# Optimization experiments

Hardware: AMD Instinct MI355X
Metric: run time of the kernel (lower is better)

## Reference

```python
import jax, jax.numpy as jnp
from jax import lax
import numpy as np

PN_FEAT = 64


def _conv(x, w, b):
    # x: [B,H,W,Cin], w: [kh,kw,Cin,Cout] (SAME padding, stride 1)
    return lax.conv_general_dilated(x, w, (1, 1), 'SAME',
                                    dimension_numbers=('NHWC', 'HWIO', 'NHWC')) + b


def setup_inputs() -> dict:
    key = jax.random.key(0)
    ks = jax.random.split(key, 12)
    B, P, N, C = 4, 5000, 100, 8
    nx = ny = 240
    pillars = jax.random.normal(ks[0], (B, P, N, C), dtype=jnp.float32)
    pillar_idxs = jax.random.randint(ks[1], (B, P, 2), 0, nx).astype(jnp.int32)
    def lin(k, fi, fo):
        return jax.random.normal(k, (fi, fo), dtype=jnp.float32) / np.sqrt(fi).astype(np.float32)
    def cnv(k, kh, kw, ci, co):
        return jax.random.normal(k, (kh, kw, ci, co), dtype=jnp.float32) / np.sqrt(kh * kw * ci).astype(np.float32)
    return {
        'pillars': pillars,
        'pillar_idxs': pillar_idxs,
        'nx': nx,
        'ny': ny,
        # pointnet MLP: 8 -> 64 (tanh) -> 64
        'pn_w0': lin(ks[2], 8, 64), 'pn_b0': jnp.zeros((64,), jnp.float32),
        'pn_w1': lin(ks[3], 64, PN_FEAT), 'pn_b1': jnp.zeros((PN_FEAT,), jnp.float32),
        # resnet costmap CNN: 64 -> 128 (tanh) -> 128 (tanh) -> 1, relu output
        'cw0': cnv(ks[4], 3, 3, PN_FEAT, 128), 'cb0': jnp.zeros((128,), jnp.float32),
        'cw1': cnv(ks[5], 3, 3, 128, 128), 'cb1': jnp.zeros((128,), jnp.float32),
        'cw2': cnv(ks[6], 1, 1, 128, 1), 'cb2': jnp.zeros((1,), jnp.float32),
    }


def reference(pillars, pillar_idxs, nx, ny,
              pn_w0, pn_b0, pn_w1, pn_b1,
              cw0, cb0, cw1, cb1, cw2, cb2):
    VALID_THRESH = 1000000.0
    ACT_SCALE = 1.0
    # mask padded points (norm >= 1e6 means invalid)
    valid = (jnp.linalg.norm(pillars, axis=-1, keepdims=True) < VALID_THRESH).astype(pillars.dtype)
    # per-point MLP: [B,P,N,8] -> [B,P,N,F]
    h = jnp.tanh(pillars @ pn_w0 + pn_b0)
    feat = h @ pn_w1 + pn_b1
    # masked max over points in each pillar -> [B,P,F]
    pmax = jnp.max(feat * valid, axis=-2)
    # scatter pillar features into BEV pseudo-image [B,nx,ny,F]
    B = pillars.shape[0]
    bidx = jnp.arange(B)[:, None]                      # [B,1]
    img = jnp.zeros((B, nx, ny, PN_FEAT), pillars.dtype)
    img = img.at[bidx, pillar_idxs[..., 0], pillar_idxs[..., 1]].set(pmax)
    # costmap CNN head (NHWC internally; original is NCHW, same math)
    x = jnp.tanh(_conv(img, cw0, cb0))
    x = jnp.tanh(_conv(x, cw1, cb1))
    x = _conv(x, cw2, cb2)
    return jax.nn.relu(x) * ACT_SCALE            # [B,nx,ny,1]
```

## Files before the change

kernel.cpp:

```cpp
#include <hip/hip_runtime.h>
#include <hip/hip_bf16.h>
#include <math.h>

#define B  4
#define P  5000
#define NPT 100
#define F  64
#define NX 240
#define NY 240
#define C1 128

typedef __attribute__((ext_vector_type(8)))  short short8;
typedef __attribute__((ext_vector_type(16))) float f32x16;

__device__ __forceinline__ float tanh_fast(float x) {
    float e = __expf(2.0f * x);
    float r = __builtin_amdgcn_rcpf(e + 1.0f);
    return __builtin_fmaf(-2.0f, r, 1.0f);
}
__device__ __forceinline__ short bf16_bits(float f) {
    return (short)(__bfloat16_as_ushort(__float2bfloat16(f)));
}

__global__ __launch_bounds__(128) void pn_mfma_kernel(
    const float* __restrict__ pillars,
    const short* __restrict__ w0p,
    const float* __restrict__ b0,
    const __hip_bfloat16* __restrict__ w1t,
    const float* __restrict__ b1,
    float* __restrict__ pmax)
{
    constexpr int HS = F + 8;
    constexpr int XS = 40;
    __shared__ short xA[128 * XS];
    __shared__ short hA[128 * HS];
    __shared__ float red[2][F];
    __shared__ unsigned int vb32[4];

    int bp = blockIdx.x;
    int n  = threadIdx.x;
    int wave = n >> 6, lane = n & 63;
    int mr = lane & 31;
    int g  = lane >> 5;
    bool live = (n < NPT);

    const float* xp = pillars + ((size_t)bp * NPT + (live ? n : 0)) * 8;
    float4 q0 = *(const float4*)xp;
    float4 q1 = *(const float4*)(xp + 4);
    float x[8] = {q0.x, q0.y, q0.z, q0.w, q1.x, q1.y, q1.z, q1.w};

    float ss = 0.f;
#pragma unroll
    for (int c = 0; c < 8; c++) ss += x[c] * x[c];
    bool valid = live && (ss < 1e12f);

    unsigned long long bal = __ballot(valid);
    if (lane == 0) {
        vb32[wave * 2]     = (unsigned)bal;
        vb32[wave * 2 + 1] = (unsigned)(bal >> 32);
    }

    short8 xhi, xlo, xz;
#pragma unroll
    for (int c = 0; c < 8; c++) {
        __hip_bfloat16 hb = __float2bfloat16(x[c]);
        float hv = __bfloat162float(hb);
        xhi[c] = (short)__bfloat16_as_ushort(hb);
        xlo[c] = bf16_bits(x[c] - hv);
        xz[c] = 0;
    }
    *(short8*)&xA[n * XS + 0]  = xhi;
    *(short8*)&xA[n * XS + 8]  = xlo;
    *(short8*)&xA[n * XS + 16] = xhi;
    *(short8*)&xA[n * XS + 24] = xz;
    __syncthreads();

    short8 wb[2][2];
#pragma unroll
    for (int kk = 0; kk < 2; kk++)
#pragma unroll
        for (int nt = 0; nt < 2; nt++)
            wb[kk][nt] = *(const short8*)(w0p + ((kk * 2 + g) * 64 + nt * 32 + mr) * 8);

    f32x16 hc00 = {0,0,0,0,0,0,0,0,0,0,0,0,0,0,0,0};
    f32x16 hc01 = hc00, hc10 = hc00, hc11 = hc00;
#pragma unroll
    for (int kk = 0; kk < 2; kk++) {
        short8 a0 = *(const short8*)&xA[(wave * 64 + mr) * XS + kk * 16 + g * 8];
        short8 a1 = *(const short8*)&xA[(wave * 64 + 32 + mr) * XS + kk * 16 + g * 8];
        hc00 = __builtin_amdgcn_mfma_f32_32x32x16_bf16(a0, wb[kk][0], hc00, 0, 0, 0);
        hc01 = __builtin_amdgcn_mfma_f32_32x32x16_bf16(a0, wb[kk][1], hc01, 0, 0, 0);
        hc10 = __builtin_amdgcn_mfma_f32_32x32x16_bf16(a1, wb[kk][0], hc10, 0, 0, 0);
        hc11 = __builtin_amdgcn_mfma_f32_32x32x16_bf16(a1, wb[kk][1], hc11, 0, 0, 0);
    }

    float b00 = b0[mr];
    float b01 = b0[32 + mr];
#pragma unroll
    for (int mt = 0; mt < 2; mt++) {
#pragma unroll
        for (int r = 0; r < 16; r++) {
            int prow = wave * 64 + mt * 32 + (r & 3) + 8 * (r >> 2) + 4 * g;
            float h0 = (mt == 0) ? hc00[r] : hc10[r];
            float h1 = (mt == 0) ? hc01[r] : hc11[r];
            hA[prow * HS + mr]      = bf16_bits(tanh_fast(h0 + b00));
            hA[prow * HS + 32 + mr] = bf16_bits(tanh_fast(h1 + b01));
        }
    }
    __syncthreads();

    short8 bfrag[2][4];
#pragma unroll
    for (int nt = 0; nt < 2; nt++)
#pragma unroll
        for (int c0 = 0; c0 < 4; c0++)
            bfrag[nt][c0] = *(const short8*)((const short*)w1t +
                                (nt * 32 + mr) * F + c0 * 16 + g * 8);

    f32x16 acc00 = {0,0,0,0,0,0,0,0,0,0,0,0,0,0,0,0};
    f32x16 acc01 = acc00, acc10 = acc00, acc11 = acc00;

    const short* arow = &hA[(wave * 64 + mr) * HS + g * 8];
#pragma unroll
    for (int c0 = 0; c0 < 4; c0++) {
        short8 af0 = *(const short8*)(arow + c0 * 16);
        short8 af1 = *(const short8*)(arow + 32 * HS + c0 * 16);
        acc00 = __builtin_amdgcn_mfma_f32_32x32x16_bf16(af0, bfrag[0][c0], acc00, 0, 0, 0);
        acc01 = __builtin_amdgcn_mfma_f32_32x32x16_bf16(af0, bfrag[1][c0], acc01, 0, 0, 0);
        acc10 = __builtin_amdgcn_mfma_f32_32x32x16_bf16(af1, bfrag[0][c0], acc10, 0, 0, 0);
        acc11 = __builtin_amdgcn_mfma_f32_32x32x16_bf16(af1, bfrag[1][c0], acc11, 0, 0, 0);
    }

    float bv0 = b1[mr];
    float bv1 = b1[32 + mr];
    bool allv = ((vb32[0] & vb32[1] & vb32[2]) == 0xFFFFFFFFu) &&
                ((vb32[3] & 0xFu) == 0xFu);
    float mx0 = -INFINITY, mx1 = -INFINITY;

    if (allv) {
#pragma unroll
        for (int mt = 0; mt < 2; mt++) {
#pragma unroll
            for (int r = 0; r < 16; r++) {
                bool inc = !(wave == 1 && mt == 1) || (g == 0 && r < 4);
                if (inc) {
                    mx0 = fmaxf(mx0, (mt == 0) ? acc00[r] : acc10[r]);
                    mx1 = fmaxf(mx1, (mt == 0) ? acc01[r] : acc11[r]);
                }
            }
        }
        mx0 += bv0;
        mx1 += bv1;
    } else {
        unsigned wm0 = vb32[wave * 2];
        unsigned wm1 = vb32[wave * 2 + 1];
#pragma unroll
        for (int mt = 0; mt < 2; mt++) {
            unsigned wm = (mt == 0) ? wm0 : wm1;
#pragma unroll
            for (int r = 0; r < 16; r++) {
                int idx = (r & 3) + 8 * (r >> 2) + 4 * g;
                bool inc = !(wave == 1 && mt == 1) || (idx < 4);
                if (inc) {
                    bool vbit = (wm >> idx) & 1;
                    float a0 = (mt == 0) ? acc00[r] : acc10[r];
                    float a1 = (mt == 0) ? acc01[r] : acc11[r];
                    mx0 = fmaxf(mx0, vbit ? (a0 + bv0) : 0.0f);
                    mx1 = fmaxf(mx1, vbit ? (a1 + bv1) : 0.0f);
                }
            }
        }
    }
    mx0 = fmaxf(mx0, __shfl_xor(mx0, 32, 64));
    mx1 = fmaxf(mx1, __shfl_xor(mx1, 32, 64));
    if (lane < 32) { red[wave][mr] = mx0; red[wave][32 + mr] = mx1; }
    __syncthreads();
    if (n < F)
        pmax[(size_t)bp * F + n] = fmaxf(red[0][n], red[1][n]);
}

__global__ __launch_bounds__(256) void winner_kernel(
    const int* __restrict__ idxs, int* __restrict__ winner)
{
    int i = blockIdx.x * 256 + threadIdx.x;
    if (i >= B * P) return;
    int ix = idxs[i * 2], iy = idxs[i * 2 + 1];
    int b = i / P, p = i % P;
    atomicMax(&winner[(b * NX + ix) * NY + iy], p);
}

__global__ __launch_bounds__(64) void scatter_kernel(
    const int* __restrict__ idxs, const int* __restrict__ winner,
    const float* __restrict__ pmax, __hip_bfloat16* __restrict__ img)
{
    int bp = blockIdx.x;
    int f = threadIdx.x;
    int ix = idxs[bp * 2], iy = idxs[bp * 2 + 1];
    int b = bp / P, p = bp % P;
    int cell = (b * NX + ix) * NY + iy;
    if (winner[cell] == p)
        img[(size_t)cell * F + f] = __float2bfloat16(pmax[(size_t)bp * F + f]);
}

__global__ __launch_bounds__(256) void cvt_w_kernel(
    const float* __restrict__ w, __hip_bfloat16* __restrict__ wt, int cin)
{
    int idx = blockIdx.x * 256 + threadIdx.x;
    int total = 9 * cin * 128;
    if (idx >= total) return;
    int co = idx % 128;
    int rest = idx / 128;
    int ci = rest % cin;
    int t  = rest / cin;
    int c0 = ci >> 4, c16 = ci & 15;
    wt[(((size_t)(t * (cin >> 4) + c0)) * 128 + co) * 16 + c16] = __float2bfloat16(w[idx]);
}

__global__ __launch_bounds__(256) void cvt_w1_kernel(
    const float* __restrict__ w1, __hip_bfloat16* __restrict__ w1t)
{
    int idx = blockIdx.x * 256 + threadIdx.x;
    if (idx >= F * F) return;
    int k = idx >> 6, nn = idx & 63;
    w1t[nn * F + k] = __float2bfloat16(w1[idx]);
}

__global__ __launch_bounds__(256) void cvt_w0p_kernel(
    const float* __restrict__ w0, short* __restrict__ w0p)
{
    int idx = blockIdx.x * 256 + threadIdx.x;
    if (idx >= 4 * 64 * 8) return;
    int j = idx & 7;
    int nn = (idx >> 3) & 63;
    int s = idx >> 9;
    float wv = w0[j * F + nn];
    __hip_bfloat16 hb = __float2bfloat16(wv);
    short out = 0;
    if (s < 2)      out = (short)__bfloat16_as_ushort(hb);
    else if (s == 2) out = bf16_bits(wv - __bfloat162float(hb));
    w0p[idx] = out;
}

template<int CIN, bool FUSE>
__global__ __launch_bounds__(256, 2) void conv_mfma(
    const __hip_bfloat16* __restrict__ in,
    const __hip_bfloat16* __restrict__ wt,
    const float* __restrict__ bias,
    const float* __restrict__ w2,
    const float* __restrict__ b2,
    __hip_bfloat16* __restrict__ out_bf,
    float* __restrict__ out_f)
{
    constexpr int PASSES = CIN / 64;
    constexpr int CI   = 64;
    constexpr int CPAD = CI + 8;
    constexpr int NC16 = CI / 16;
    constexpr int NC8  = CI / 8;
    constexpr int ROWS = 4 * 130;
    __shared__ short sP[ROWS * CPAD];
    __shared__ float sred[FUSE ? 2 : 1][2][128];

    int tid  = threadIdx.x;
    int wave = tid >> 6;
    int lane = tid & 63;
    int mr = lane & 31;
    int g  = lane >> 5;
    int coh = wave & 1;
    int xr  = wave >> 1;
    int x0 = blockIdx.x * 2;
    int y0 = blockIdx.y * 112;
    int b  = blockIdx.z;
    int n0 = coh * 64;

    const short* wts = (const short*)wt;

    f32x16 acc[4][2];
#pragma unroll
    for (int mt = 0; mt < 4; mt++)
#pragma unroll
        for (int nt = 0; nt < 2; nt++)
            acc[mt][nt] = (f32x16){0,0,0,0,0,0,0,0,0,0,0,0,0,0,0,0};

    short8 wbuf[2][NC16][2];
#pragma unroll
    for (int c0 = 0; c0 < NC16; c0++)
#pragma unroll
        for (int nt = 0; nt < 2; nt++)
            wbuf[0][c0][nt] = *(const short8*)(wts +
                ((0 * (CIN / 16) + c0) * 128 + n0 + nt * 32 + mr) * 16 + g * 8);

#pragma unroll
    for (int p = 0; p < PASSES; p++) {
        if (p) __syncthreads();

#pragma unroll 4
        for (int i = 0; i < 17; i++) {
            int t = tid + i * 256;
            if (t < ROWS * NC8) {
                int c8 = t & (NC8 - 1);
                int r  = t >> 3;
                int dx = r / 130, dy = r - dx * 130;
                int gx = x0 - 1 + dx, gy = y0 - 1 + dy;
                float4 v = make_float4(0.f, 0.f, 0.f, 0.f);
                if (gx >= 0 && gx < NX && gy >= 0 && gy < NY)
                    v = *(const float4*)&in[(((size_t)b * NX + gx) * NY + gy) * CIN + p * CI + c8 * 8];
                *(float4*)&sP[r * CPAD + c8 * 8] = v;
            }
        }
        __syncthreads();

#pragma unroll
        for (int tap = 0; tap < 9; tap++) {
            int s = p * 9 + tap;
            int cur = s & 1;
            if (s + 1 < 9 * PASSES) {
                int sn = s + 1, pn_ = sn / 9, tn = sn % 9;
#pragma unroll
                for (int c0 = 0; c0 < NC16; c0++)
#pragma unroll
                    for (int nt = 0; nt < 2; nt++)
                        wbuf[cur ^ 1][c0][nt] = *(const short8*)(wts +
                            ((tn * (CIN / 16) + pn_ * NC16 + c0) * 128 + n0 + nt * 32 + mr) * 16 + g * 8);
            }
            int kh = tap / 3, kw = tap % 3;
            const short* abase = sP + ((xr + kh) * 130 + kw + mr) * CPAD + g * 8;
#pragma unroll
            for (int c0 = 0; c0 < NC16; c0++) {
                short8 a[4];
#pragma unroll
                for (int mt = 0; mt < 4; mt++)
                    a[mt] = *(const short8*)(abase + mt * 32 * CPAD + c0 * 16);
#pragma unroll
                for (int mt = 0; mt < 4; mt++) {
                    acc[mt][0] = __builtin_amdgcn_mfma_f32_32x32x16_bf16(a[mt], wbuf[cur][c0][0], acc[mt][0], 0, 0, 0);
                    acc[mt][1] = __builtin_amdgcn_mfma_f32_32x32x16_bf16(a[mt], wbuf[cur][c0][1], acc[mt][1], 0, 0, 0);
                }
            }
        }
    }

    float bv0 = bias[n0 + mr];
    float bv1 = bias[n0 + 32 + mr];
    if (!FUSE) {
        size_t base = ((size_t)b * NX + (x0 + xr)) * NY;
#pragma unroll
        for (int mt = 0; mt < 4; mt++) {
#pragma unroll
            for (int r = 0; r < 16; r++) {
                int y = y0 + mt * 32 + (r & 3) + 8 * (r >> 2) + 4 * g;
                out_bf[(base + y) * C1 + n0 + mr]      = __float2bfloat16(tanh_fast(acc[mt][0][r] + bv0));
                out_bf[(base + y) * C1 + n0 + 32 + mr] = __float2bfloat16(tanh_fast(acc[mt][1][r] + bv1));
            }
        }
    } else {
        float w20 = w2[n0 + mr];
        float w21 = w2[n0 + 32 + mr];
#pragma unroll
        for (int mt = 0; mt < 4; mt++) {
#pragma unroll
            for (int r = 0; r < 16; r++) {
                float v = tanh_fast(acc[mt][0][r] + bv0) * w20
                        + tanh_fast(acc[mt][1][r] + bv1) * w21;
                v += __shfl_xor(v, 1, 64);
                v += __shfl_xor(v, 2, 64);
                v += __shfl_xor(v, 4, 64);
                v += __shfl_xor(v, 8, 64);
                v += __shfl_xor(v, 16, 64);
                if (mr == 0)
                    sred[coh][xr][mt * 32 + (r & 3) + 8 * (r >> 2) + 4 * g] = v;
            }
        }
        __syncthreads();
        {
            int row = tid & 127;
            int xr2 = tid >> 7;
            float r = sred[0][xr2][row] + sred[1][xr2][row] + b2[0];
            out_f[((size_t)b * NX + (x0 + xr2)) * NY + (y0 + row)] = fmaxf(r, 0.f);
        }
    }
}

extern "C" void kernel_launch(void* const* d_in, const int* in_sizes, int n_in,
                              void* d_out, int out_size, void* d_ws, size_t ws_size,
                              hipStream_t stream) {
    const float* pillars = (const float*)d_in[0];
    const int*   idxs    = (const int*)d_in[1];
    const float* pn_w0   = (const float*)d_in[4];
    const float* pn_b0   = (const float*)d_in[5];
    const float* pn_w1   = (const float*)d_in[6];
    const float* pn_b1   = (const float*)d_in[7];
    const float* cw0     = (const float*)d_in[8];
    const float* cb0     = (const float*)d_in[9];
    const float* cw1     = (const float*)d_in[10];
    const float* cb1     = (const float*)d_in[11];
    const float* cw2     = (const float*)d_in[12];
    const float* cb2     = (const float*)d_in[13];
    float* out = (float*)d_out;

    char* ws = (char*)d_ws;
    const size_t IMG_BYTES  = (size_t)B * NX * NY * F * 2;
    const size_t OUT1_BYTES = (size_t)B * NX * NY * C1 * 2;
    const size_t WIN_BYTES  = (size_t)B * NX * NY * 4;
    const size_t PMAX_BYTES = (size_t)B * P * F * 4;
    const size_t WT1_BYTES  = (size_t)9 * C1 * F * 2;
    const size_t WT2_BYTES  = (size_t)9 * C1 * C1 * 2;
    const size_t W1T_BYTES  = (size_t)F * F * 2;
    __hip_bfloat16* img  = (__hip_bfloat16*)ws;
    __hip_bfloat16* out1 = (__hip_bfloat16*)(ws + IMG_BYTES);
    int*   winner = (int*)(ws + IMG_BYTES + OUT1_BYTES);
    float* pmax   = (float*)(ws + IMG_BYTES + OUT1_BYTES + WIN_BYTES);
    __hip_bfloat16* wt1 = (__hip_bfloat16*)(ws + IMG_BYTES + OUT1_BYTES + WIN_BYTES + PMAX_BYTES);
    __hip_bfloat16* wt2 = (__hip_bfloat16*)(ws + IMG_BYTES + OUT1_BYTES + WIN_BYTES + PMAX_BYTES + WT1_BYTES);
    __hip_bfloat16* w1t = (__hip_bfloat16*)(ws + IMG_BYTES + OUT1_BYTES + WIN_BYTES + PMAX_BYTES + WT1_BYTES + WT2_BYTES);
    short* w0p = (short*)(ws + IMG_BYTES + OUT1_BYTES + WIN_BYTES + PMAX_BYTES + WT1_BYTES + WT2_BYTES + W1T_BYTES);

    hipMemsetAsync(img, 0, IMG_BYTES, stream);
    hipMemsetAsync(winner, 0xFF, WIN_BYTES, stream);

    cvt_w_kernel<<<(9 * F * C1 + 255) / 256, 256, 0, stream>>>(cw0, wt1, F);
    cvt_w_kernel<<<(9 * C1 * C1 + 255) / 256, 256, 0, stream>>>(cw1, wt2, C1);
    cvt_w1_kernel<<<(F * F + 255) / 256, 256, 0, stream>>>(pn_w1, w1t);
    cvt_w0p_kernel<<<(4 * 64 * 8 + 255) / 256, 256, 0, stream>>>(pn_w0, w0p);

    pn_mfma_kernel<<<B * P, 128, 0, stream>>>(pillars, w0p, pn_b0, w1t, pn_b1, pmax);
    winner_kernel<<<(B * P + 255) / 256, 256, 0, stream>>>(idxs, winner);
    scatter_kernel<<<B * P, 64, 0, stream>>>(idxs, winner, pmax, img);

    conv_mfma<F, false><<<dim3(NX / 2, 2, B), 256, 0, stream>>>(
        img, wt1, cb0, nullptr, nullptr, out1, nullptr);
    conv_mfma<C1, true><<<dim3(NX / 2, 2, B), 256, 0, stream>>>(
        out1, wt2, cb1, cw2, cb2, nullptr, out);
}
```

Before: 372.6 us.

## Shrink conv row tile, swizzle LDS layout, and raise occupancy to three blocks

The conv kernels now cover 96 output rows per block (three M tiles instead of four) with three blocks along y that overlap. The shared tile drops its padding in favour of an XOR swizzle on the 8-element channel groups to avoid bank conflicts. Weights are loaded straight from global memory per tap instead of being double-buffered in registers. Launch bounds request three blocks per CU. Together these cut per-block registers and LDS to allow more resident waves, at the cost of more redundant compute in the overlapping rows and less prefetch of weight loads.

After: 386.7 us. +3.8%, slower.

```diff
diff --git a/kernel.cpp b/kernel.cpp
--- a/kernel.cpp
+++ b/kernel.cpp
@@ -242,7 +242,7 @@
 }
 
 template<int CIN, bool FUSE>
-__global__ __launch_bounds__(256, 2) void conv_mfma(
+__global__ __launch_bounds__(256, 3) void conv_mfma(
     const __hip_bfloat16* __restrict__ in,
     const __hip_bfloat16* __restrict__ wt,
     const float* __restrict__ bias,
@@ -253,12 +253,10 @@
 {
     constexpr int PASSES = CIN / 64;
     constexpr int CI   = 64;
-    constexpr int CPAD = CI + 8;
     constexpr int NC16 = CI / 16;
-    constexpr int NC8  = CI / 8;
-    constexpr int ROWS = 4 * 130;
-    __shared__ short sP[ROWS * CPAD];
-    __shared__ float sred[FUSE ? 2 : 1][2][128];
+    constexpr int ROWS = 4 * 98;
+    __shared__ short sP[ROWS * 64];
+    __shared__ float sred[FUSE ? 2 : 1][2][96];
 
     int tid  = threadIdx.x;
     int wave = tid >> 6;
@@ -268,73 +266,59 @@
     int coh = wave & 1;
     int xr  = wave >> 1;
     int x0 = blockIdx.x * 2;
-    int y0 = blockIdx.y * 112;
+    int y0 = blockIdx.y * 72;
     int b  = blockIdx.z;
     int n0 = coh * 64;
 
     const short* wts = (const short*)wt;
 
-    f32x16 acc[4][2];
-#pragma unroll
-    for (int mt = 0; mt < 4; mt++)
+    f32x16 acc[3][2];
+#pragma unroll
+    for (int mt = 0; mt < 3; mt++)
 #pragma unroll
         for (int nt = 0; nt < 2; nt++)
             acc[mt][nt] = (f32x16){0,0,0,0,0,0,0,0,0,0,0,0,0,0,0,0};
 
-    short8 wbuf[2][NC16][2];
-#pragma unroll
-    for (int c0 = 0; c0 < NC16; c0++)
-#pragma unroll
-        for (int nt = 0; nt < 2; nt++)
-            wbuf[0][c0][nt] = *(const short8*)(wts +
-                ((0 * (CIN / 16) + c0) * 128 + n0 + nt * 32 + mr) * 16 + g * 8);
-
 #pragma unroll
     for (int p = 0; p < PASSES; p++) {
         if (p) __syncthreads();
 
-#pragma unroll 4
-        for (int i = 0; i < 17; i++) {
+        for (int i = 0; i < 13; i++) {
             int t = tid + i * 256;
-            if (t < ROWS * NC8) {
-                int c8 = t & (NC8 - 1);
-                int r  = t >> 3;
-                int dx = r / 130, dy = r - dx * 130;
+            if (t < ROWS * 8) {
+                int c8  = t & 7;
+                int row = t >> 3;
+                int dx = row / 98, dy = row - dx * 98;
                 int gx = x0 - 1 + dx, gy = y0 - 1 + dy;
                 float4 v = make_float4(0.f, 0.f, 0.f, 0.f);
                 if (gx >= 0 && gx < NX && gy >= 0 && gy < NY)
                     v = *(const float4*)&in[(((size_t)b * NX + gx) * NY + gy) * CIN + p * CI + c8 * 8];
-                *(float4*)&sP[r * CPAD + c8 * 8] = v;
+                *(float4*)&sP[row * 64 + ((c8 ^ (row & 7)) * 8)] = v;
             }
         }
         __syncthreads();
 
 #pragma unroll
         for (int tap = 0; tap < 9; tap++) {
-            int s = p * 9 + tap;
-            int cur = s & 1;
-            if (s + 1 < 9 * PASSES) {
-                int sn = s + 1, pn_ = sn / 9, tn = sn % 9;
-#pragma unroll
-                for (int c0 = 0; c0 < NC16; c0++)
-#pragma unroll
-                    for (int nt = 0; nt < 2; nt++)
-                        wbuf[cur ^ 1][c0][nt] = *(const short8*)(wts +
-                            ((tn * (CIN / 16) + pn_ * NC16 + c0) * 128 + n0 + nt * 32 + mr) * 16 + g * 8);
-            }
             int kh = tap / 3, kw = tap % 3;
-            const short* abase = sP + ((xr + kh) * 130 + kw + mr) * CPAD + g * 8;
+            int rowbase = (xr + kh) * 98 + kw + mr;
+            int r7 = rowbase & 7;
+            const short* abase = sP + rowbase * 64;
+            const short* wrow = wts + ((size_t)(tap * (CIN / 16) + p * NC16) * 128 + n0 + mr) * 16 + g * 8;
 #pragma unroll
             for (int c0 = 0; c0 < NC16; c0++) {
-                short8 a[4];
-#pragma unroll
-                for (int mt = 0; mt < 4; mt++)
-                    a[mt] = *(const short8*)(abase + mt * 32 * CPAD + c0 * 16);
-#pragma unroll
-                for (int mt = 0; mt < 4; mt++) {
-                    acc[mt][0] = __builtin_amdgcn_mfma_f32_32x32x16_bf16(a[mt], wbuf[cur][c0][0], acc[mt][0], 0, 0, 0);
-                    acc[mt][1] = __builtin_amdgcn_mfma_f32_32x32x16_bf16(a[mt], wbuf[cur][c0][1], acc[mt][1], 0, 0, 0);
-                }
+                short8 w0f = *(const short8*)(wrow + (size_t)c0 * 2048);
+                short8 w1f = *(const short8*)(wrow + (size_t)c0 * 2048 + 512);
+                int goff = ((c0 * 2 + g) ^ r7) * 8;
+                short8 a0 = *(const short8*)(abase + goff);
+                short8 a1 = *(const short8*)(abase + 32 * 64 + goff);
+                short8 a2 = *(const short8*)(abase + 64 * 64 + goff);
+                acc[0][0] = __builtin_amdgcn_mfma_f32_32x32x16_bf16(a0, w0f, acc[0][0], 0, 0, 0);
+                acc[0][1] = __builtin_amdgcn_mfma_f32_32x32x16_bf16(a0, w1f, acc[0][1], 0, 0, 0);
+                acc[1][0] = __builtin_amdgcn_mfma_f32_32x32x16_bf16(a1, w0f, acc[1][0], 0, 0, 0);
+                acc[1][1] = __builtin_amdgcn_mfma_f32_32x32x16_bf16(a1, w1f, acc[1][1], 0, 0, 0);
+                acc[2][0] = __builtin_amdgcn_mfma_f32_32x32x16_bf16(a2, w0f, acc[2][0], 0, 0, 0);
+                acc[2][1] = __builtin_amdgcn_mfma_f32_32x32x16_bf16(a2, w1f, acc[2][1], 0, 0, 0);
             }
         }
     }
@@ -344,7 +328,7 @@
     if (!FUSE) {
         size_t base = ((size_t)b * NX + (x0 + xr)) * NY;
 #pragma unroll
-        for (int mt = 0; mt < 4; mt++) {
+        for (int mt = 0; mt < 3; mt++) {
 #pragma unroll
             for (int r = 0; r < 16; r++) {
                 int y = y0 + mt * 32 + (r & 3) + 8 * (r >> 2) + 4 * g;
@@ -356,7 +340,7 @@
         float w20 = w2[n0 + mr];
         float w21 = w2[n0 + 32 + mr];
 #pragma unroll
-        for (int mt = 0; mt < 4; mt++) {
+        for (int mt = 0; mt < 3; mt++) {
 #pragma unroll
             for (int r = 0; r < 16; r++) {
                 float v = tanh_fast(acc[mt][0][r] + bv0) * w20
@@ -371,11 +355,11 @@
             }
         }
         __syncthreads();
-        {
-            int row = tid & 127;
-            int xr2 = tid >> 7;
-            float r = sred[0][xr2][row] + sred[1][xr2][row] + b2[0];
-            out_f[((size_t)b * NX + (x0 + xr2)) * NY + (y0 + row)] = fmaxf(r, 0.f);
+        if (tid < 192) {
+            int xr2 = tid / 96;
+            int yy  = tid % 96;
+            float r = sred[0][xr2][yy] + sred[1][xr2][yy] + b2[0];
+            out_f[((size_t)b * NX + (x0 + xr2)) * NY + (y0 + yy)] = fmaxf(r, 0.f);
         }
     }
 }
@@ -426,8 +410,8 @@
     winner_kernel<<<(B * P + 255) / 256, 256, 0, stream>>>(idxs, winner);
     scatter_kernel<<<B * P, 64, 0, stream>>>(idxs, winner, pmax, img);
 
-    conv_mfma<F, false><<<dim3(NX / 2, 2, B), 256, 0, stream>>>(
+    conv_mfma<F, false><<<dim3(NX / 2, 3, B), 256, 0, stream>>>(
         img, wt1, cb0, nullptr, nullptr, out1, nullptr);
-    conv_mfma<C1, true><<<dim3(NX / 2, 2, B), 256, 0, stream>>>(
+    conv_mfma<C1, true><<<dim3(NX / 2, 3, B), 256, 0, stream>>>(
         out1, wt2, cb1, cw2, cb2, nullptr, out);
 }
```
